# Optimization experiments

Measured on AMD Instinct MI355X. Metric: run time of the kernel, lower is better.

## Reference

```python
import jax, jax.numpy as jnp
import numpy as np

NUM_HEADS = 16
ROPE_BASE = 10000.0
QK_GAIN_INIT = 12.0
EPS = 1e-6
# head_config = alternating ['rope','nope',...]; 1.0 -> RoPE applied to this head
ROPE_MASK = jnp.asarray(np.tile([1.0, 0.0], NUM_HEADS // 2), dtype=jnp.float32)


def setup_inputs() -> dict:
    key = jax.random.key(0)
    k0, k1, k2 = jax.random.split(key, 3)
    B, S, Dm = 2, 2048, 2048
    x = jax.random.normal(k0, (B, S, Dm), dtype=jnp.float32)
    # fused QKV projection and output projection (out_proj flagged zero-init in the
    # original; we use small random init so outputs/grads are non-trivial)
    w_qkv = jax.random.normal(k1, (Dm, 3 * Dm), dtype=jnp.float32) * (Dm ** -0.5)
    w_out = jax.random.normal(k2, (Dm, Dm), dtype=jnp.float32) * (Dm ** -0.5)
    q_gain = jnp.full((NUM_HEADS,), QK_GAIN_INIT, dtype=jnp.float32)
    return {"x": x, "w_qkv": w_qkv, "w_out": w_out, "q_gain": q_gain}


def _rope_cos_sin(seqlen, head_dim, dtype):
    half = head_dim // 2
    inv_freq = ROPE_BASE ** (-jnp.arange(0, half, dtype=jnp.float32) / half)
    theta = jnp.arange(seqlen, dtype=jnp.float32)[:, None] * inv_freq[None, :]  # [S, D/2]
    return jnp.cos(theta).astype(dtype), jnp.sin(theta).astype(dtype)


def _apply_rope(t, cos, sin):
    # t: [B, S, H, D]; cos/sin: [S, D/2] -> broadcast [1, S, 1, D/2]
    d2 = t.shape[-1] // 2
    t1, t2 = t[..., :d2], t[..., d2:]
    c = cos[None, :, None, :]
    s = sin[None, :, None, :]
    return jnp.concatenate([t1 * c - t2 * s, t1 * s + t2 * c], axis=-1)


def _unit_norm(t):
    # per-head-dim L2 normalization (qk-norm)
    return t * jax.lax.rsqrt(jnp.sum(t * t, axis=-1, keepdims=True) + EPS)


def reference(x, w_qkv, w_out, q_gain):
    B, S, Dm = x.shape
    H = NUM_HEADS
    D = Dm // H
    qkv = (x @ w_qkv).reshape(B, S, 3, H, D)
    q, k, v = qkv[:, :, 0], qkv[:, :, 1], qkv[:, :, 2]  # [B, S, H, D]
    q = _unit_norm(q)
    k = _unit_norm(k)
    cos, sin = _rope_cos_sin(S, D, x.dtype)
    m = ROPE_MASK[None, None, :, None]  # heterogeneous per-head dispatch
    q = m * _apply_rope(q, cos, sin) + (1.0 - m) * q
    k = m * _apply_rope(k, cos, sin) + (1.0 - m) * k
    # per-head learned qk gain instead of 1/sqrt(d)
    logits = jnp.einsum('bshd,bthd->bhst', q, k) * q_gain[None, :, None, None]
    causal = jnp.tril(jnp.ones((S, S), dtype=bool))
    logits = jnp.where(causal[None, None], logits, jnp.finfo(logits.dtype).min)
    attn = jax.nn.softmax(logits, axis=-1)
    y = jnp.einsum('bhst,bthd->bshd', attn, v).reshape(B, S, Dm)
    return y @ w_out
```

## Files before the change

kernel.cpp:

```cpp
#include <hip/hip_runtime.h>
#include <hip/hip_bf16.h>

typedef unsigned short ushort_t;
typedef __attribute__((ext_vector_type(8))) short short8;
typedef __attribute__((ext_vector_type(4))) float floatx4;

#define B_  2
#define S_  2048
#define DM_ 2048
#define H_  16
#define DH_ 128

#define AS1(p) ((const __attribute__((address_space(1))) void*)(p))
#define AS3(p) ((__attribute__((address_space(3))) void*)(p))

static __device__ __forceinline__ float b2f(ushort_t u) {
  __hip_bfloat16 h = *reinterpret_cast<__hip_bfloat16*>(&u);
  return __bfloat162float(h);
}
static __device__ __forceinline__ ushort_t f2b(float f) {
  __hip_bfloat16 h = __float2bfloat16(f);
  return *reinterpret_cast<ushort_t*>(&h);
}
static __device__ __forceinline__ float fast_exp2(float x) {
#if defined(__has_builtin)
#if __has_builtin(__builtin_amdgcn_exp2f)
  return __builtin_amdgcn_exp2f(x);
#else
  return exp2f(x);
#endif
#else
  return exp2f(x);
#endif
}

__global__ __launch_bounds__(256) void convert_f32_bf16(const float* __restrict__ in,
                                                        ushort_t* __restrict__ out) {
  size_t i = ((size_t)blockIdx.x * 256 + threadIdx.x) * 8;
  float4 a = *(const float4*)(in + i);
  float4 b = *(const float4*)(in + i + 4);
  ushort_t tmp[8] = {f2b(a.x), f2b(a.y), f2b(a.z), f2b(a.w),
                     f2b(b.x), f2b(b.y), f2b(b.z), f2b(b.w)};
  *(uint4*)(out + i) = *(const uint4*)tmp;
}

__global__ __launch_bounds__(256) void transpose_f32_to_bf16T(const float* __restrict__ in,
                                                              ushort_t* __restrict__ out,
                                                              int R, int inC, int colOff) {
  __shared__ ushort_t tile[64][72];
  const int tid = threadIdx.x;
  const int r0 = blockIdx.y * 64, c0 = blockIdx.x * 64;
#pragma unroll
  for (int p = 0; p < 2; ++p) {
    int li = tid + p * 256;
    int r = li >> 3, cs = (li & 7) * 8;
    const float* src = in + (size_t)(r0 + r) * inC + colOff + c0 + cs;
    float4 a = *(const float4*)src;
    float4 b = *(const float4*)(src + 4);
    ushort_t tmp[8] = {f2b(a.x), f2b(a.y), f2b(a.z), f2b(a.w),
                       f2b(b.x), f2b(b.y), f2b(b.z), f2b(b.w)};
    *(uint4*)&tile[r][cs] = *(const uint4*)tmp;
  }
  __syncthreads();
#pragma unroll
  for (int p = 0; p < 2; ++p) {
    int li = tid + p * 256;
    int cR = li >> 3, rs = (li & 7) * 8;
    ushort_t tmp[8];
#pragma unroll
    for (int e = 0; e < 8; ++e) tmp[e] = tile[rs + e][cR];
    *(uint4*)(out + (size_t)(c0 + cR) * R + r0 + rs) = *(const uint4*)tmp;
  }
}

#define SBAR() __builtin_amdgcn_sched_barrier(0)
#define BARR() __builtin_amdgcn_s_barrier()

#define LDS_A(qm, bb)                                                          \
  _Pragma("unroll") for (int mi = 0; mi < 4; ++mi) {                           \
    _Pragma("unroll") for (int ks = 0; ks < 2; ++ks) {                         \
      const int r_ = arow + (qm) * 64 + mi * 16;                               \
      const int cb_ = ((ks) * 64 + quad * 16) ^ swz;                           \
      afr[qm][mi][ks] =                                                        \
          *(const short8*)((const char*)As[bb] + r_ * 128 + cb_);              \
    }                                                                          \
  }

#define LDS_B(qn, bb)                                                          \
  _Pragma("unroll") for (int ni = 0; ni < 2; ++ni) {                           \
    _Pragma("unroll") for (int ks = 0; ks < 2; ++ks) {                         \
      const int r_ = brow + (qn) * 32 + ni * 16;                               \
      const int cb_ = ((ks) * 64 + quad * 16) ^ swz;                           \
      bfr[qn][ni][ks] =                                                        \
          *(const short8*)((const char*)Bs[bb] + r_ * 128 + cb_);              \
    }                                                                          \
  }

#define MMA_Q(qm, qn)                                                          \
  _Pragma("unroll") for (int mi = 0; mi < 4; ++mi) {                           \
    _Pragma("unroll") for (int ni = 0; ni < 2; ++ni) {                         \
      floatx4 t_ = acc[(qm) * 4 + mi][(qn) * 2 + ni];                          \
      t_ = __builtin_amdgcn_mfma_f32_16x16x32_bf16(afr[qm][mi][0],             \
                                                   bfr[qn][ni][0], t_, 0, 0, 0); \
      t_ = __builtin_amdgcn_mfma_f32_16x16x32_bf16(afr[qm][mi][1],             \
                                                   bfr[qn][ni][1], t_, 0, 0, 0); \
      acc[(qm) * 4 + mi][(qn) * 2 + ni] = t_;                                  \
    }                                                                          \
  }

template <int MODE>
__global__ __launch_bounds__(512, 2) void gemm_bt_256(const ushort_t* __restrict__ A,
                                                      const ushort_t* __restrict__ Bt,
                                                      void* __restrict__ C0,
                                                      void* __restrict__ C1,
                                                      int M, int N, int K) {
  __shared__ alignas(16) ushort_t As[2][256 * 64];
  __shared__ alignas(16) ushort_t Bs[2][256 * 64];
  const int tid = threadIdx.x;
  const int wave = tid >> 6, lane = tid & 63;
  const int l15 = lane & 15, quad = lane >> 4;
  const int wm = wave >> 2, wn = wave & 3;
  const size_t m0 = (size_t)blockIdx.y * 256, n0 = (size_t)blockIdx.x * 256;
  const int nkt = K >> 6;

  const int srow = lane >> 3;
  const int skk = ((lane & 7) ^ srow) * 8;

  const int arow = wm * 128 + l15;
  const int brow = wn * 64 + l15;
  const int swz = (l15 & 7) << 4;

  floatx4 zero = {0.f, 0.f, 0.f, 0.f};
  floatx4 acc[8][4];
#pragma unroll
  for (int i = 0; i < 8; ++i)
#pragma unroll
    for (int j = 0; j < 4; ++j) acc[i][j] = zero;

  short8 afr[2][4][2];
  short8 bfr[2][2][2];

  auto stage_half = [&](int t, int ht) {
    if (t >= nkt) return;
    const int bb = t & 1;
    const int h = ht & 1;
    const int kt64 = t << 6;
    const ushort_t* G = (ht < 2) ? A : Bt;
    const size_t r0 = (ht < 2) ? m0 : n0;
    char* dst = (char*)((ht < 2) ? As[bb] : Bs[bb]) + h * 16384;
#pragma unroll
    for (int i = 0; i < 2; ++i) {
      const int c = wave * 2 + i;
      const size_t gr = r0 + h * 128 + c * 8 + srow;
      __builtin_amdgcn_global_load_lds(AS1(G + gr * K + kt64 + skk),
                                       AS3(dst + c * 1024), 16, 0, 0);
    }
  };

  stage_half(0, 0); stage_half(0, 1); stage_half(0, 2); stage_half(0, 3);
  stage_half(1, 0); stage_half(1, 1);
  SBAR();
  if (nkt > 1) { asm volatile("s_waitcnt vmcnt(4)" ::: "memory"); }
  else         { asm volatile("s_waitcnt vmcnt(0)" ::: "memory"); }
  SBAR(); BARR(); SBAR();

  for (int kt = 0; kt < nkt; ++kt) {
    const int bb = kt & 1;
    LDS_A(0, bb); LDS_B(0, bb);
    stage_half(kt + 1, 2);
    SBAR(); BARR(); SBAR();
    __builtin_amdgcn_s_setprio(1);
    MMA_Q(0, 0);
    __builtin_amdgcn_s_setprio(0);
    SBAR(); BARR(); SBAR();
    LDS_A(1, bb);
    stage_half(kt + 1, 3);
    SBAR(); BARR(); SBAR();
    __builtin_amdgcn_s_setprio(1);
    MMA_Q(1, 0);
    __builtin_amdgcn_s_setprio(0);
    SBAR(); BARR(); SBAR();
    LDS_B(1, bb);
    stage_half(kt + 2, 0);
    SBAR(); BARR(); SBAR();
    __builtin_amdgcn_s_setprio(1);
    MMA_Q(1, 1);
    __builtin_amdgcn_s_setprio(0);
    SBAR(); BARR(); SBAR();
    stage_half(kt + 2, 1);
    SBAR(); BARR(); SBAR();
    __builtin_amdgcn_s_setprio(1);
    MMA_Q(0, 1);
    __builtin_amdgcn_s_setprio(0);
    SBAR();
    if (kt + 2 < nkt) { asm volatile("s_waitcnt vmcnt(4)" ::: "memory"); }
    else              { asm volatile("s_waitcnt vmcnt(0)" ::: "memory"); }
    SBAR(); BARR(); SBAR();
  }

  if (MODE == 2) {
    ushort_t* Cb = (n0 >= 2048) ? (ushort_t*)C1 : (ushort_t*)C0;
    size_t nc0 = n0 & 2047;
#pragma unroll
    for (int mi8 = 0; mi8 < 8; ++mi8)
#pragma unroll
      for (int nj = 0; nj < 4; ++nj)
#pragma unroll
        for (int r = 0; r < 4; ++r) {
          size_t row = m0 + wm * 128 + (mi8 >> 2) * 64 + (mi8 & 3) * 16 + quad * 4 + r;
          size_t col = nc0 + wn * 64 + (nj >> 1) * 32 + (nj & 1) * 16 + l15;
          Cb[row * 2048 + col] = f2b(acc[mi8][nj][r]);
        }
  } else {
#pragma unroll
    for (int mi8 = 0; mi8 < 8; ++mi8)
#pragma unroll
      for (int nj = 0; nj < 4; ++nj)
#pragma unroll
        for (int r = 0; r < 4; ++r) {
          size_t row = m0 + wm * 128 + (mi8 >> 2) * 64 + (mi8 & 3) * 16 + quad * 4 + r;
          size_t col = n0 + wn * 64 + (nj >> 1) * 32 + (nj & 1) * 16 + l15;
          if (MODE == 1)
            ((float*)C0)[row * N + col] = acc[mi8][nj][r];
          else
            ((ushort_t*)C0)[row * N + col] = f2b(acc[mi8][nj][r]);
        }
  }
}

#define LDS_A8(mh, bb)                                                         \
  _Pragma("unroll") for (int mi = 0; mi < 2; ++mi) {                           \
    _Pragma("unroll") for (int ks = 0; ks < 2; ++ks) {                         \
      const int r_ = arow + ((mh) * 2 + mi) * 16;                              \
      const int cb_ = ((ks) * 64 + quad * 16) ^ swz;                           \
      afr[(mh) * 2 + mi][ks] =                                                 \
          *(const short8*)((const char*)As[bb] + r_ * 128 + cb_);              \
    }                                                                          \
  }

#define LDS_B8(nh, bb)                                                         \
  _Pragma("unroll") for (int ni = 0; ni < 2; ++ni) {                           \
    _Pragma("unroll") for (int ks = 0; ks < 2; ++ks) {                         \
      const int r_ = brow + ((nh) * 2 + ni) * 16;                              \
      const int cb_ = ((ks) * 64 + quad * 16) ^ swz;                           \
      bfr[(nh) * 2 + ni][ks] =                                                 \
          *(const short8*)((const char*)Bs[bb] + r_ * 128 + cb_);              \
    }                                                                          \
  }

#define MMA_H(mh, nh)                                                          \
  _Pragma("unroll") for (int mi = 0; mi < 2; ++mi) {                           \
    _Pragma("unroll") for (int ni = 0; ni < 2; ++ni) {                         \
      floatx4 t_ = acc[(mh) * 2 + mi][(nh) * 2 + ni];                          \
      t_ = __builtin_amdgcn_mfma_f32_16x16x32_bf16(afr[(mh) * 2 + mi][0],      \
                                                   bfr[(nh) * 2 + ni][0], t_, 0, 0, 0); \
      t_ = __builtin_amdgcn_mfma_f32_16x16x32_bf16(afr[(mh) * 2 + mi][1],      \
                                                   bfr[(nh) * 2 + ni][1], t_, 0, 0, 0); \
      acc[(mh) * 2 + mi][(nh) * 2 + ni] = t_;                                  \
    }                                                                          \
  }

template <int MODE>
__global__ __launch_bounds__(256, 2) void gemm_bt_128(const ushort_t* __restrict__ A,
                                                      const ushort_t* __restrict__ Bt,
                                                      void* __restrict__ C0,
                                                      int M, int N, int K) {
  __shared__ alignas(16) ushort_t As[2][128 * 64];
  __shared__ alignas(16) ushort_t Bs[2][128 * 64];
  const int tid = threadIdx.x;
  const int wave = tid >> 6, lane = tid & 63;
  const int l15 = lane & 15, quad = lane >> 4;
  const int wm = wave >> 1, wn = wave & 1;
  const int lin = blockIdx.y * gridDim.x + blockIdx.x;
  const int band = lin / (4 * gridDim.x);
  const int rin = lin % (4 * gridDim.x);
  const int by = band * 4 + (rin & 3);
  const int bx = rin >> 2;
  const size_t m0 = (size_t)by * 128, n0 = (size_t)bx * 128;
  const int nkt = K >> 6;

  const int srow = lane >> 3;
  const int skk = ((lane & 7) ^ srow) * 8;

  const int arow = wm * 64 + l15;
  const int brow = wn * 64 + l15;
  const int swz = (l15 & 7) << 4;

  floatx4 zero = {0.f, 0.f, 0.f, 0.f};
  floatx4 acc[4][4];
#pragma unroll
  for (int i = 0; i < 4; ++i)
#pragma unroll
    for (int j = 0; j < 4; ++j) acc[i][j] = zero;

  short8 afr[4][2];
  short8 bfr[4][2];

  auto stage_q = [&](int t, int qt_) {
    if (t >= nkt) return;
    const int bb = t & 1;
    const int h = qt_ & 1;
    const int kt64 = t << 6;
    const ushort_t* G = (qt_ < 2) ? A : Bt;
    const size_t r0 = (qt_ < 2) ? m0 : n0;
    char* dst = (char*)((qt_ < 2) ? As[bb] : Bs[bb]) + h * 8192;
#pragma unroll
    for (int i = 0; i < 2; ++i) {
      const int c = wave * 2 + i;
      const size_t gr = r0 + h * 64 + c * 8 + srow;
      __builtin_amdgcn_global_load_lds(AS1(G + gr * K + kt64 + skk),
                                       AS3(dst + c * 1024), 16, 0, 0);
    }
  };

  stage_q(0, 0); stage_q(0, 1); stage_q(0, 2); stage_q(0, 3);
  stage_q(1, 0); stage_q(1, 1);
  SBAR();
  if (nkt > 1) { asm volatile("s_waitcnt vmcnt(4)" ::: "memory"); }
  else         { asm volatile("s_waitcnt vmcnt(0)" ::: "memory"); }
  SBAR(); BARR(); SBAR();

  for (int kt = 0; kt < nkt; ++kt) {
    const int bb = kt & 1;
    LDS_A8(0, bb); LDS_B8(0, bb);
    stage_q(kt + 1, 2);
    SBAR(); BARR(); SBAR();
    __builtin_amdgcn_s_setprio(1);
    MMA_H(0, 0);
    __builtin_amdgcn_s_setprio(0);
    SBAR(); BARR(); SBAR();
    LDS_A8(1, bb);
    stage_q(kt + 1, 3);
    SBAR(); BARR(); SBAR();
    __builtin_amdgcn_s_setprio(1);
    MMA_H(1, 0);
    __builtin_amdgcn_s_setprio(0);
    SBAR(); BARR(); SBAR();
    LDS_B8(1, bb);
    stage_q(kt + 2, 0);
    SBAR(); BARR(); SBAR();
    __builtin_amdgcn_s_setprio(1);
    MMA_H(1, 1);
    __builtin_amdgcn_s_setprio(0);
    SBAR(); BARR(); SBAR();
    stage_q(kt + 2, 1);
    SBAR(); BARR(); SBAR();
    __builtin_amdgcn_s_setprio(1);
    MMA_H(0, 1);
    __builtin_amdgcn_s_setprio(0);
    SBAR();
    if (kt + 2 < nkt) { asm volatile("s_waitcnt vmcnt(4)" ::: "memory"); }
    else              { asm volatile("s_waitcnt vmcnt(0)" ::: "memory"); }
    SBAR(); BARR(); SBAR();
  }

#pragma unroll
  for (int i = 0; i < 4; ++i)
#pragma unroll
    for (int j = 0; j < 4; ++j)
#pragma unroll
      for (int r = 0; r < 4; ++r) {
        size_t row = m0 + wm * 64 + i * 16 + quad * 4 + r;
        size_t col = n0 + wn * 64 + j * 16 + l15;
        if (MODE == 1)
          ((float*)C0)[row * N + col] = acc[i][j][r];
        else
          ((ushort_t*)C0)[row * N + col] = f2b(acc[i][j][r]);
      }
}

__global__ __launch_bounds__(256) void norm_rope(ushort_t* __restrict__ Q,
                                                 ushort_t* __restrict__ Kb,
                                                 const float* __restrict__ gain) {
  const int tid = threadIdx.x;
  const int wave = tid >> 6, lane = tid & 63;
  const int g16 = lane >> 4, sl = lane & 15;
  const int idx = (blockIdx.x * 4 + wave) * 4 + g16;
  const int h = idx & 15;
  const int s = (idx >> 4) & (S_ - 1);
  const size_t off = (size_t)(idx >> 4) * DM_ + h * DH_ + sl * 4;

  ushort_t qv1[4], qv2[4], kv1[4], kv2[4];
  *(uint2*)qv1 = *(const uint2*)(Q + off);
  *(uint2*)qv2 = *(const uint2*)(Q + off + 64);
  *(uint2*)kv1 = *(const uint2*)(Kb + off);
  *(uint2*)kv2 = *(const uint2*)(Kb + off + 64);

  float q1[4], q2[4], k1[4], k2[4];
  float sq = 0.f, sk = 0.f;
#pragma unroll
  for (int e = 0; e < 4; ++e) {
    q1[e] = b2f(qv1[e]); q2[e] = b2f(qv2[e]);
    k1[e] = b2f(kv1[e]); k2[e] = b2f(kv2[e]);
    sq += q1[e] * q1[e] + q2[e] * q2[e];
    sk += k1[e] * k1[e] + k2[e] * k2[e];
  }
#pragma unroll
  for (int o = 1; o < 16; o <<= 1) {
    sq += __shfl_xor(sq, o, 64);
    sk += __shfl_xor(sk, o, 64);
  }
  float rq = rsqrtf(sq + 1e-6f), rk = rsqrtf(sk + 1e-6f);
  const float g = gain[h] * 1.44269504f;
  const bool roped = (h & 1) == 0;
#pragma unroll
  for (int e = 0; e < 4; ++e) {
    float a = q1[e] * rq, bq = q2[e] * rq;
    float c_ = k1[e] * rk, dk = k2[e] * rk;
    if (roped) {
      int j = sl * 4 + e;
      float invf = exp2f((float)j * -0.20762050593f);
      float th = (float)s * invf;
      float cc = cosf(th), sn = sinf(th);
      float na = a * cc - bq * sn, nb = a * sn + bq * cc;
      float nc = c_ * cc - dk * sn, nd = c_ * sn + dk * cc;
      a = na; bq = nb; c_ = nc; dk = nd;
    }
    qv1[e] = f2b(a * g); qv2[e] = f2b(bq * g);
    kv1[e] = f2b(c_);    kv2[e] = f2b(dk);
  }
  *(uint2*)(Q + off)       = *(const uint2*)qv1;
  *(uint2*)(Q + off + 64)  = *(const uint2*)qv2;
  *(uint2*)(Kb + off)      = *(const uint2*)kv1;
  *(uint2*)(Kb + off + 64) = *(const uint2*)kv2;
}

__global__ __launch_bounds__(256, 2) void attn(ushort_t* __restrict__ QY,
                                               const ushort_t* __restrict__ Kg,
                                               const ushort_t* __restrict__ Vg) {
  __shared__ alignas(16) ushort_t Ks[2][64 * 128];
  __shared__ alignas(16) ushort_t Vs[2][128 * 64];
  __shared__ alignas(16) ushort_t Ps[2][4][16 * 64];

  const float M0 = 18.755035531f;
  const int tid = threadIdx.x;
  const int wave = tid >> 6, lane = tid & 63;
  const int l15 = lane & 15, quad = lane >> 4;
  const int bh = blockIdx.x;
  const int b = bh >> 4, h = bh & 15;
  const int p = blockIdx.y;
  const int qt[2] = {p, 31 - p};

  const ushort_t* Kgb = Kg + (size_t)b * S_ * DM_ + h * DH_;
  const ushort_t* Vgb = Vg + (size_t)(h * DH_) * (B_ * S_) + b * S_;

  short8 aq[2][4];
#pragma unroll
  for (int t = 0; t < 2; ++t) {
    const ushort_t* Qg =
        QY + (size_t)(b * S_ + qt[t] * 64 + wave * 16 + l15) * DM_ + h * DH_;
#pragma unroll
    for (int ks = 0; ks < 4; ++ks)
      aq[t][ks] = *(const short8*)(Qg + ks * 32 + quad * 8);
  }

  float lsum[2][4] = {{0.f, 0.f, 0.f, 0.f}, {0.f, 0.f, 0.f, 0.f}};
  floatx4 zero = {0.f, 0.f, 0.f, 0.f};
  floatx4 oacc[2][8];
#pragma unroll
  for (int t = 0; t < 2; ++t)
#pragma unroll
    for (int d = 0; d < 8; ++d) oacc[t][d] = zero;

  const int krow_in = lane >> 4, ksd = lane & 15;
  const int vrow_in = lane >> 3, vsd = lane & 7;

  auto stage = [&](int kt, int bf) {
#pragma unroll
    for (int i = 0; i < 4; ++i) {
      int c = wave * 4 + i;
      {
        int r = c * 4 + krow_in;
        int sg = ksd ^ (r & 7);
        __builtin_amdgcn_global_load_lds(
            AS1(Kgb + (size_t)(kt * 64 + r) * DM_ + sg * 8),
            AS3((char*)Ks[bf] + c * 1024), 16, 0, 0);
      }
      {
        int r = c * 8 + vrow_in;
        int sg = vsd ^ (r & 7);
        __builtin_amdgcn_global_load_lds(
            AS1(Vgb + (size_t)r * (B_ * S_) + kt * 64 + sg * 8),
            AS3((char*)Vs[bf] + c * 1024), 16, 0, 0);
      }
    }
  };

  stage(0, 0);

  for (int kt = 0; kt <= qt[1]; ++kt) {
    const int cur = kt & 1;
    __syncthreads();
    if (kt < qt[1]) stage(kt + 1, cur ^ 1);

#pragma unroll
    for (int t = 0; t < 2; ++t) {
      if (t == 0 && kt > qt[0]) continue;
      floatx4 sacc[4];
#pragma unroll
      for (int j = 0; j < 4; ++j) sacc[j] = zero;
#pragma unroll
      for (int ks = 0; ks < 4; ++ks) {
#pragma unroll
        for (int j = 0; j < 4; ++j) {
          int row = j * 16 + l15;
          int sl = (ks * 4 + quad) ^ (row & 7);
          short8 bk = *(const short8*)&Ks[cur][row * 128 + sl * 8];
          sacc[j] = __builtin_amdgcn_mfma_f32_16x16x32_bf16(aq[t][ks], bk, sacc[j], 0, 0, 0);
        }
      }
      if (kt == qt[t]) {
#pragma unroll
        for (int j = 0; j < 4; ++j)
#pragma unroll
          for (int r = 0; r < 4; ++r) {
            int key = j * 16 + l15;
            int qr = wave * 16 + quad * 4 + r;
            if (key > qr) sacc[j][r] = -1e30f;
          }
      }
#pragma unroll
      for (int j = 0; j < 4; ++j)
#pragma unroll
        for (int r = 0; r < 4; ++r) {
          float pv = fast_exp2(sacc[j][r] - M0);
          sacc[j][r] = pv;
          lsum[t][r] += pv;
        }
#pragma unroll
      for (int j = 0; j < 4; ++j)
#pragma unroll
        for (int r = 0; r < 4; ++r) {
          int row = quad * 4 + r;
          int col = j * 16 + l15;
          int g = col >> 3, w = col & 7;
          Ps[t][wave][row * 64 + ((g ^ (row & 7)) << 3) + w] = f2b(sacc[j][r]);
        }
#pragma unroll
      for (int ks2 = 0; ks2 < 2; ++ks2) {
        short8 ap = *(const short8*)&Ps[t][wave][l15 * 64 +
                                                (((ks2 * 4 + quad) ^ (l15 & 7)) << 3)];
#pragma unroll
        for (int d = 0; d < 8; ++d) {
          int row = d * 16 + l15;
          int sl = (ks2 * 4 + quad) ^ (row & 7);
          short8 bv = *(const short8*)&Vs[cur][row * 64 + sl * 8];
          oacc[t][d] = __builtin_amdgcn_mfma_f32_16x16x32_bf16(ap, bv, oacc[t][d], 0, 0, 0);
        }
      }
    }
  }

#pragma unroll
  for (int t = 0; t < 2; ++t) {
#pragma unroll
    for (int r = 0; r < 4; ++r) {
#pragma unroll
      for (int o = 1; o < 16; o <<= 1) lsum[t][r] += __shfl_xor(lsum[t][r], o, 64);
      float inv = 1.0f / lsum[t][r];
      size_t row = (size_t)(b * S_ + qt[t] * 64 + wave * 16 + quad * 4 + r);
#pragma unroll
      for (int d = 0; d < 8; ++d) {
        size_t col = (size_t)h * DH_ + d * 16 + l15;
        QY[row * DM_ + col] = f2b(oacc[t][d][r] * inv);
      }
    }
  }
}

extern "C" void kernel_launch(void* const* d_in, const int* in_sizes, int n_in,
                              void* d_out, int out_size, void* d_ws, size_t ws_size,
                              hipStream_t stream) {
  const float* x      = (const float*)d_in[0];
  const float* w_qkv  = (const float*)d_in[1];
  const float* w_out  = (const float*)d_in[2];
  const float* q_gain = (const float*)d_in[3];
  float* out = (float*)d_out;

  char* ws = (char*)d_ws;
  const size_t bsd = (size_t)B_ * S_ * DM_;
  ushort_t* Qraw = (ushort_t*)ws;
  ushort_t* Kraw = Qraw + bsd;
  ushort_t* Vt   = Kraw + bsd;
  ushort_t* wvT  = Vt + bsd;
  ushort_t* xbf  = (ushort_t*)d_out;
  ushort_t* wqkT = xbf + bsd;
  ushort_t* woutT = Kraw;

  convert_f32_bf16<<<dim3(bsd / (8 * 256)), 256, 0, stream>>>(x, xbf);
  transpose_f32_to_bf16T<<<dim3(64, 32), 256, 0, stream>>>(w_qkv, wqkT, DM_, 3 * DM_, 0);
  transpose_f32_to_bf16T<<<dim3(32, 32), 256, 0, stream>>>(w_qkv, wvT, DM_, 3 * DM_, 2 * DM_);

  gemm_bt_256<2><<<dim3(16, 16), 512, 0, stream>>>(xbf, wqkT, Qraw, Kraw,
                                                   B_ * S_, 2 * DM_, DM_);
  gemm_bt_128<0><<<dim3(32, 16), 256, 0, stream>>>(wvT, xbf, Vt,
                                                   DM_, B_ * S_, DM_);
  norm_rope<<<dim3(B_ * S_ * H_ / 16), 256, 0, stream>>>(Qraw, Kraw, q_gain);
  attn<<<dim3(B_ * H_, S_ / 128), 256, 0, stream>>>(Qraw, Kraw, Vt);
  transpose_f32_to_bf16T<<<dim3(32, 32), 256, 0, stream>>>(w_out, woutT, DM_, DM_, 0);
  gemm_bt_128<1><<<dim3(16, 32), 256, 0, stream>>>(Qraw, woutT, out,
                                                   B_ * S_, DM_, DM_);
}
```

Before: 363.8 us.

## Drop redundant barriers in GEMM main loops and merge w_qkv transpose launches

Removes the workgroup barrier placed between each LDS-load/stage step and the following MFMA block in both GEMM kernels, keeping only compiler scheduling barriers. Waves can then start their MFMAs without waiting for every other wave, which is meant to cut stall time in the pipelined main loop. It also merges the two w_qkv transpose launches into one 3D-grid kernel to save a launch. The risk is that the removed barriers were guarding LDS reuse between waves, which could introduce races.

Measured after the change: 352.6 us. 1.03x faster.

```diff
diff --git a/kernel.cpp b/kernel.cpp
--- a/kernel.cpp
+++ b/kernel.cpp
@@ -47,6 +47,40 @@
 __global__ __launch_bounds__(256) void transpose_f32_to_bf16T(const float* __restrict__ in,
                                                               ushort_t* __restrict__ out,
                                                               int R, int inC, int colOff) {
+  __shared__ ushort_t tile[64][72];
+  const int tid = threadIdx.x;
+  const int r0 = blockIdx.y * 64, c0 = blockIdx.x * 64;
+#pragma unroll
+  for (int p = 0; p < 2; ++p) {
+    int li = tid + p * 256;
+    int r = li >> 3, cs = (li & 7) * 8;
+    const float* src = in + (size_t)(r0 + r) * inC + colOff + c0 + cs;
+    float4 a = *(const float4*)src;
+    float4 b = *(const float4*)(src + 4);
+    ushort_t tmp[8] = {f2b(a.x), f2b(a.y), f2b(a.z), f2b(a.w),
+                       f2b(b.x), f2b(b.y), f2b(b.z), f2b(b.w)};
+    *(uint4*)&tile[r][cs] = *(const uint4*)tmp;
+  }
+  __syncthreads();
+#pragma unroll
+  for (int p = 0; p < 2; ++p) {
+    int li = tid + p * 256;
+    int cR = li >> 3, rs = (li & 7) * 8;
+    ushort_t tmp[8];
+#pragma unroll
+    for (int e = 0; e < 8; ++e) tmp[e] = tile[rs + e][cR];
+    *(uint4*)(out + (size_t)(c0 + cR) * R + r0 + rs) = *(const uint4*)tmp;
+  }
+}
+
+__global__ __launch_bounds__(256) void transpose_wqkv(const float* __restrict__ in,
+                                                      ushort_t* __restrict__ outQK,
+                                                      ushort_t* __restrict__ outV) {
+  const int z = blockIdx.z;
+  if (z == 1 && blockIdx.x >= 32) return;
+  ushort_t* out = z ? outV : outQK;
+  const int colOff = z ? 2 * DM_ : 0;
+  const int R = DM_, inC = 3 * DM_;
   __shared__ ushort_t tile[64][72];
   const int tid = threadIdx.x;
   const int r0 = blockIdx.y * 64, c0 = blockIdx.x * 64;
@@ -168,27 +202,27 @@
     const int bb = kt & 1;
     LDS_A(0, bb); LDS_B(0, bb);
     stage_half(kt + 1, 2);
-    SBAR(); BARR(); SBAR();
+    SBAR();
     __builtin_amdgcn_s_setprio(1);
     MMA_Q(0, 0);
     __builtin_amdgcn_s_setprio(0);
     SBAR(); BARR(); SBAR();
     LDS_A(1, bb);
     stage_half(kt + 1, 3);
-    SBAR(); BARR(); SBAR();
+    SBAR();
     __builtin_amdgcn_s_setprio(1);
     MMA_Q(1, 0);
     __builtin_amdgcn_s_setprio(0);
     SBAR(); BARR(); SBAR();
     LDS_B(1, bb);
     stage_half(kt + 2, 0);
-    SBAR(); BARR(); SBAR();
+    SBAR();
     __builtin_amdgcn_s_setprio(1);
     MMA_Q(1, 1);
     __builtin_amdgcn_s_setprio(0);
     SBAR(); BARR(); SBAR();
     stage_half(kt + 2, 1);
-    SBAR(); BARR(); SBAR();
+    SBAR();
     __builtin_amdgcn_s_setprio(1);
     MMA_Q(0, 1);
     __builtin_amdgcn_s_setprio(0);
@@ -324,27 +358,27 @@
     const int bb = kt & 1;
     LDS_A8(0, bb); LDS_B8(0, bb);
     stage_q(kt + 1, 2);
-    SBAR(); BARR(); SBAR();
+    SBAR();
     __builtin_amdgcn_s_setprio(1);
     MMA_H(0, 0);
     __builtin_amdgcn_s_setprio(0);
     SBAR(); BARR(); SBAR();
     LDS_A8(1, bb);
     stage_q(kt + 1, 3);
-    SBAR(); BARR(); SBAR();
+    SBAR();
     __builtin_amdgcn_s_setprio(1);
     MMA_H(1, 0);
     __builtin_amdgcn_s_setprio(0);
     SBAR(); BARR(); SBAR();
     LDS_B8(1, bb);
     stage_q(kt + 2, 0);
-    SBAR(); BARR(); SBAR();
+    SBAR();
     __builtin_amdgcn_s_setprio(1);
     MMA_H(1, 1);
     __builtin_amdgcn_s_setprio(0);
     SBAR(); BARR(); SBAR();
     stage_q(kt + 2, 1);
-    SBAR(); BARR(); SBAR();
+    SBAR();
     __builtin_amdgcn_s_setprio(1);
     MMA_H(0, 1);
     __builtin_amdgcn_s_setprio(0);
@@ -588,8 +622,7 @@
   ushort_t* woutT = Kraw;
 
   convert_f32_bf16<<<dim3(bsd / (8 * 256)), 256, 0, stream>>>(x, xbf);
-  transpose_f32_to_bf16T<<<dim3(64, 32), 256, 0, stream>>>(w_qkv, wqkT, DM_, 3 * DM_, 0);
-  transpose_f32_to_bf16T<<<dim3(32, 32), 256, 0, stream>>>(w_qkv, wvT, DM_, 3 * DM_, 2 * DM_);
+  transpose_wqkv<<<dim3(64, 32, 2), 256, 0, stream>>>(w_qkv, wqkT, wvT);
 
   gemm_bt_256<2><<<dim3(16, 16), 512, 0, stream>>>(xbf, wqkT, Qraw, Kraw,
                                                    B_ * S_, 2 * DM_, DM_);
```

## Fuse prep kernels and cut barriers in GEMM main loops

Applied to the files above, without the earlier changes.

Merges the x conversion and both w_qkv transposes into one launch, and folds the w_out transpose into the norm/rope launch, writing woutT into the wvT buffer, which is free by then. This removes several kernel launches and lets the transpose overlap with norm work. In both GEMM kernels the LDS fragment loads are reordered so more fragments are read before the MMAs, and four of the block barriers per iteration are removed. Fewer barriers risk LDS buffer hazards, and the earlier fragment loads raise register pressure.

Result: faster. 350.0 us (-3.8%).

```diff
diff --git a/kernel.cpp b/kernel.cpp
--- a/kernel.cpp
+++ b/kernel.cpp
@@ -34,22 +34,12 @@
 #endif
 }
 
-__global__ __launch_bounds__(256) void convert_f32_bf16(const float* __restrict__ in,
-                                                        ushort_t* __restrict__ out) {
-  size_t i = ((size_t)blockIdx.x * 256 + threadIdx.x) * 8;
-  float4 a = *(const float4*)(in + i);
-  float4 b = *(const float4*)(in + i + 4);
-  ushort_t tmp[8] = {f2b(a.x), f2b(a.y), f2b(a.z), f2b(a.w),
-                     f2b(b.x), f2b(b.y), f2b(b.z), f2b(b.w)};
-  *(uint4*)(out + i) = *(const uint4*)tmp;
-}
-
-__global__ __launch_bounds__(256) void transpose_f32_to_bf16T(const float* __restrict__ in,
-                                                              ushort_t* __restrict__ out,
-                                                              int R, int inC, int colOff) {
-  __shared__ ushort_t tile[64][72];
-  const int tid = threadIdx.x;
-  const int r0 = blockIdx.y * 64, c0 = blockIdx.x * 64;
+static __device__ __forceinline__ void transpose_body(const float* __restrict__ in,
+                                                      ushort_t* __restrict__ out,
+                                                      int R, int inC, int colOff,
+                                                      int bx, int by,
+                                                      ushort_t (*tile)[72], int tid) {
+  const int r0 = by * 64, c0 = bx * 64;
 #pragma unroll
   for (int p = 0; p < 2; ++p) {
     int li = tid + p * 256;
@@ -70,6 +60,32 @@
 #pragma unroll
     for (int e = 0; e < 8; ++e) tmp[e] = tile[rs + e][cR];
     *(uint4*)(out + (size_t)(c0 + cR) * R + r0 + rs) = *(const uint4*)tmp;
+  }
+}
+
+__global__ __launch_bounds__(256) void fused_pre(const float* __restrict__ x,
+                                                 const float* __restrict__ w_qkv,
+                                                 ushort_t* __restrict__ xbf,
+                                                 ushort_t* __restrict__ wqkT,
+                                                 ushort_t* __restrict__ wvT) {
+  __shared__ ushort_t tile[64][72];
+  const int bid = blockIdx.x;
+  const int tid = threadIdx.x;
+  if (bid < 4096) {
+    size_t i = ((size_t)bid * 256 + tid) * 8;
+    float4 a = *(const float4*)(x + i);
+    float4 b = *(const float4*)(x + i + 4);
+    ushort_t tmp[8] = {f2b(a.x), f2b(a.y), f2b(a.z), f2b(a.w),
+                       f2b(b.x), f2b(b.y), f2b(b.z), f2b(b.w)};
+    *(uint4*)(xbf + i) = *(const uint4*)tmp;
+    return;
+  }
+  if (bid < 6144) {
+    int t = bid - 4096;
+    transpose_body(w_qkv, wqkT, DM_, 3 * DM_, 0, t & 63, t >> 6, tile, tid);
+  } else {
+    int t = bid - 6144;
+    transpose_body(w_qkv, wvT, DM_, 3 * DM_, 2 * DM_, t & 31, t >> 5, tile, tid);
   }
 }
 
@@ -166,29 +182,28 @@
 
   for (int kt = 0; kt < nkt; ++kt) {
     const int bb = kt & 1;
-    LDS_A(0, bb); LDS_B(0, bb);
+    LDS_A(0, bb); LDS_B(0, bb); LDS_A(1, bb);
     stage_half(kt + 1, 2);
-    SBAR(); BARR(); SBAR();
+    SBAR();
     __builtin_amdgcn_s_setprio(1);
     MMA_Q(0, 0);
     __builtin_amdgcn_s_setprio(0);
     SBAR(); BARR(); SBAR();
-    LDS_A(1, bb);
+    LDS_B(1, bb);
     stage_half(kt + 1, 3);
-    SBAR(); BARR(); SBAR();
+    SBAR();
     __builtin_amdgcn_s_setprio(1);
     MMA_Q(1, 0);
     __builtin_amdgcn_s_setprio(0);
     SBAR(); BARR(); SBAR();
-    LDS_B(1, bb);
     stage_half(kt + 2, 0);
-    SBAR(); BARR(); SBAR();
+    SBAR();
     __builtin_amdgcn_s_setprio(1);
     MMA_Q(1, 1);
     __builtin_amdgcn_s_setprio(0);
     SBAR(); BARR(); SBAR();
     stage_half(kt + 2, 1);
-    SBAR(); BARR(); SBAR();
+    SBAR();
     __builtin_amdgcn_s_setprio(1);
     MMA_Q(0, 1);
     __builtin_amdgcn_s_setprio(0);
@@ -322,29 +337,28 @@
 
   for (int kt = 0; kt < nkt; ++kt) {
     const int bb = kt & 1;
-    LDS_A8(0, bb); LDS_B8(0, bb);
+    LDS_A8(0, bb); LDS_B8(0, bb); LDS_A8(1, bb);
     stage_q(kt + 1, 2);
-    SBAR(); BARR(); SBAR();
+    SBAR();
     __builtin_amdgcn_s_setprio(1);
     MMA_H(0, 0);
     __builtin_amdgcn_s_setprio(0);
     SBAR(); BARR(); SBAR();
-    LDS_A8(1, bb);
+    LDS_B8(1, bb);
     stage_q(kt + 1, 3);
-    SBAR(); BARR(); SBAR();
+    SBAR();
     __builtin_amdgcn_s_setprio(1);
     MMA_H(1, 0);
     __builtin_amdgcn_s_setprio(0);
     SBAR(); BARR(); SBAR();
-    LDS_B8(1, bb);
     stage_q(kt + 2, 0);
-    SBAR(); BARR(); SBAR();
+    SBAR();
     __builtin_amdgcn_s_setprio(1);
     MMA_H(1, 1);
     __builtin_amdgcn_s_setprio(0);
     SBAR(); BARR(); SBAR();
     stage_q(kt + 2, 1);
-    SBAR(); BARR(); SBAR();
+    SBAR();
     __builtin_amdgcn_s_setprio(1);
     MMA_H(0, 1);
     __builtin_amdgcn_s_setprio(0);
@@ -369,13 +383,22 @@
       }
 }
 
-__global__ __launch_bounds__(256) void norm_rope(ushort_t* __restrict__ Q,
+__global__ __launch_bounds__(256) void fused_mid(ushort_t* __restrict__ Q,
                                                  ushort_t* __restrict__ Kb,
-                                                 const float* __restrict__ gain) {
+                                                 const float* __restrict__ gain,
+                                                 const float* __restrict__ w_out,
+                                                 ushort_t* __restrict__ woutT) {
+  __shared__ ushort_t tile[64][72];
+  const int bid = blockIdx.x;
   const int tid = threadIdx.x;
+  if (bid >= 4096) {
+    int t = bid - 4096;
+    transpose_body(w_out, woutT, DM_, DM_, 0, t & 31, t >> 5, tile, tid);
+    return;
+  }
   const int wave = tid >> 6, lane = tid & 63;
   const int g16 = lane >> 4, sl = lane & 15;
-  const int idx = (blockIdx.x * 4 + wave) * 4 + g16;
+  const int idx = (bid * 4 + wave) * 4 + g16;
   const int h = idx & 15;
   const int s = (idx >> 4) & (S_ - 1);
   const size_t off = (size_t)(idx >> 4) * DM_ + h * DH_ + sl * 4;
@@ -585,19 +608,15 @@
   ushort_t* wvT  = Vt + bsd;
   ushort_t* xbf  = (ushort_t*)d_out;
   ushort_t* wqkT = xbf + bsd;
-  ushort_t* woutT = Kraw;
-
-  convert_f32_bf16<<<dim3(bsd / (8 * 256)), 256, 0, stream>>>(x, xbf);
-  transpose_f32_to_bf16T<<<dim3(64, 32), 256, 0, stream>>>(w_qkv, wqkT, DM_, 3 * DM_, 0);
-  transpose_f32_to_bf16T<<<dim3(32, 32), 256, 0, stream>>>(w_qkv, wvT, DM_, 3 * DM_, 2 * DM_);
-
+  ushort_t* woutT = wvT;
+
+  fused_pre<<<dim3(7168), 256, 0, stream>>>(x, w_qkv, xbf, wqkT, wvT);
   gemm_bt_256<2><<<dim3(16, 16), 512, 0, stream>>>(xbf, wqkT, Qraw, Kraw,
                                                    B_ * S_, 2 * DM_, DM_);
   gemm_bt_128<0><<<dim3(32, 16), 256, 0, stream>>>(wvT, xbf, Vt,
                                                    DM_, B_ * S_, DM_);
-  norm_rope<<<dim3(B_ * S_ * H_ / 16), 256, 0, stream>>>(Qraw, Kraw, q_gain);
+  fused_mid<<<dim3(5120), 256, 0, stream>>>(Qraw, Kraw, q_gain, w_out, woutT);
   attn<<<dim3(B_ * H_, S_ / 128), 256, 0, stream>>>(Qraw, Kraw, Vt);
-  transpose_f32_to_bf16T<<<dim3(32, 32), 256, 0, stream>>>(w_out, woutT, DM_, DM_, 0);
   gemm_bt_128<1><<<dim3(16, 32), 256, 0, stream>>>(Qraw, woutT, out,
                                                    B_ * S_, DM_, DM_);
 }
```
